# Optimization experiments

Hardware: AMD Instinct MI355X
Metric: run time of the kernel (lower is better)

## Reference

```python
import jax, jax.numpy as jnp
import numpy as np
import math

EPS = 1e-5
V_TH = 1.0


def heaviside(u):
    return (u >= 0.0).astype(u.dtype)


def setup_inputs() -> dict:
    key = jax.random.key(0)
    ks = jax.random.split(key, 8)
    N, C, T = 1024, 80, 500
    Cp1 = C + 1  # conv height: C + 2*32 - 64 + 1
    num_classes = 3
    x = jax.random.normal(ks[0], (N, C, T), dtype=jnp.float32)
    # Conv2d(1,1,(64,1)) params
    fan_in = 64 * 1
    bound = 1.0 / math.sqrt(fan_in)
    conv_w = jax.random.uniform(ks[1], (1, 1, 64, 1), jnp.float32, -bound, bound)
    conv_b = jax.random.uniform(ks[2], (1,), jnp.float32, -bound, bound)
    # BatchNorm1d(81), eval mode
    bn_gamma = jnp.ones((Cp1,), jnp.float32)
    bn_beta = jnp.zeros((Cp1,), jnp.float32)
    bn_mean = jax.random.normal(ks[3], (Cp1,), jnp.float32) * 0.1
    bn_var = jax.random.uniform(ks[4], (Cp1,), jnp.float32, 0.5, 1.5)
    # PLIF learnable time constant: tau = exp(-0.5)+1 -> w = -log(tau-1) = 0.5
    plif_w = jnp.asarray(0.5, jnp.float32)
    # Linear(81 -> 3)
    bnd = 1.0 / math.sqrt(Cp1)
    fc_w = jax.random.uniform(ks[5], (num_classes, Cp1), jnp.float32, -bnd, bnd)
    fc_b = jax.random.uniform(ks[6], (num_classes,), jnp.float32, -bnd, bnd)
    return {"x": x, "conv_w": conv_w, "conv_b": conv_b, "bn_gamma": bn_gamma,
            "bn_beta": bn_beta, "bn_mean": bn_mean, "bn_var": bn_var,
            "plif_w": plif_w, "fc_w": fc_w, "fc_b": fc_b}


def reference(x, conv_w, conv_b, bn_gamma, bn_beta, bn_mean, bn_var, plif_w, fc_w, fc_b):
    # x: (N, C, T) -> (N, 1, C, T), conv kernel (64,1) with padding (32,0) -> height C+1
    y = jax.lax.conv_general_dilated(x[:, None], conv_w, window_strides=(1, 1),
                                     padding=((32, 32), (0, 0)))
    y = y + conv_b[None, :, None, None]
    y = y[:, 0]  # (N, C+1, T)
    # BatchNorm1d (eval): per-channel affine normalize
    inv = bn_gamma / jnp.sqrt(bn_var + EPS)
    y = y * inv[None, :, None] + (bn_beta - bn_mean * inv)[None, :, None]
    seq = jnp.transpose(y, (2, 0, 1))  # (T, N, C+1)
    decay = jax.nn.sigmoid(plif_w)  # 1/tau
    v0 = jnp.zeros(seq.shape[1:], seq.dtype)

    def step(v, xt):
        v = v + (xt - v) * decay           # PLIF charge (decay_input, v_reset=0)
        s = heaviside(v - V_TH)            # fire
        v = v * (1.0 - s)                  # hard reset to 0
        return v, s

    _, spikes = jax.lax.scan(step, v0, seq)  # (T, N, C+1)
    feat = jnp.mean(spikes, axis=0)          # (N, C+1)
    out = feat @ fc_w.T + fc_b               # (N, num_classes); dropout = identity (eval)
    return out
```

## Files before the change

kernel.cpp:

```cpp
#include <hip/hip_runtime.h>
#include <math.h>


#define NTH      640
#define NFIR     512
#define CPW      11
#define TC       64
#define XROWS    151
#define YSTRIDE  65
#define NCHUNK   8
#define T_LEN    500
#define C_OUT    81

__global__ __launch_bounds__(NTH)
void snn_fused_ps_kernel(const float* __restrict__ x,
                         const float* __restrict__ conv_w,
                         const float* __restrict__ conv_b,
                         const float* __restrict__ bn_gamma,
                         const float* __restrict__ bn_beta,
                         const float* __restrict__ bn_mean,
                         const float* __restrict__ bn_var,
                         const float* __restrict__ plif_w,
                         const float* __restrict__ fc_w,
                         const float* __restrict__ fc_b,
                         float* __restrict__ out)
{
    __shared__ float xs[2][XROWS * TC];
    __shared__ float ybuf[2][C_OUT * YSTRIDE];
    __shared__ float wsh[64];
    __shared__ float feat[C_OUT];

    const int tid  = threadIdx.x;
    const int n    = blockIdx.x;
    const float* xn = x + (size_t)n * (80 * T_LEN);

    if (tid < 64) wsh[tid] = conv_w[tid];

    for (int i = tid; i < 32 * TC; i += NTH) { xs[0][i] = 0.0f; xs[1][i] = 0.0f; }
    for (int i = tid; i < (XROWS - 112) * TC; i += NTH) {
        xs[0][112 * TC + i] = 0.0f; xs[1][112 * TC + i] = 0.0f;
    }
    for (int i = tid; i < 1280; i += NTH) {
        const int cr = i >> 4, t4 = i & 15;
        float4 v4 = *reinterpret_cast<const float4*>(xn + cr * T_LEN + t4 * 4);
        *reinterpret_cast<float4*>(&xs[0][(cr + 32) * TC + t4 * 4]) = v4;
    }

    float v = 0.0f, cnt = 0.0f, inv_c = 0.0f, bb_c = 0.0f, decay = 0.0f;
    if (tid >= NFIR) {
        const int ch = tid - NFIR;
        decay = 1.0f / (1.0f + expf(-plif_w[0]));
        if (ch < C_OUT) {
            inv_c = bn_gamma[ch] * rsqrtf(bn_var[ch] + 1e-5f);
            bb_c  = conv_b[0] * inv_c + bn_beta[ch] - bn_mean[ch] * inv_c;
        }
    }
    __syncthreads();

    for (int c = 0; c < NCHUNK; ++c) {
        const int b = c & 1;

        if (tid < NFIR) {
            const int lane = tid & 63;
            const int co0  = (tid >> 6) * CPW;
            const float* xsb = xs[b];

            float acc[CPW];
            float win[CPW];
            #pragma unroll
            for (int r = 0; r < CPW; ++r) acc[r] = 0.0f;
            const int base = co0 * TC + lane;
            #pragma unroll
            for (int m = 0; m < CPW - 1; ++m) win[m] = xsb[base + m * TC];
            #pragma unroll
            for (int k = 0; k < 64; ++k) {
                win[(k + CPW - 1) % CPW] = xsb[base + (k + CPW - 1) * TC];
                const float wk = wsh[k];
                #pragma unroll
                for (int r = 0; r < CPW; ++r)
                    acc[r] = fmaf(wk, win[(k + r) % CPW], acc[r]);
            }
            #pragma unroll
            for (int r = 0; r < CPW; ++r) {
                const int co = co0 + r;
                if (co < C_OUT) ybuf[b][co * YSTRIDE + lane] = acc[r];
            }
        } else {
            const int sid = tid - NFIR;

            if (c < NCHUNK - 1) {
                const int t0n = (c + 1) * TC;
                float4 pf[10];
                #pragma unroll
                for (int s = 0; s < 10; ++s) {
                    const int i  = s * 128 + sid;
                    const int cr = i >> 4, t4 = i & 15;
                    int toff = t0n + t4 * 4;
                    if (toff > 496) toff = 496;
                    pf[s] = *reinterpret_cast<const float4*>(xn + cr * T_LEN + toff);
                }
                #pragma unroll
                for (int s = 0; s < 10; ++s) {
                    const int i  = s * 128 + sid;
                    const int cr = i >> 4, t4 = i & 15;
                    *reinterpret_cast<float4*>(&xs[b ^ 1][(cr + 32) * TC + t4 * 4]) = pf[s];
                }
            }

            if (c > 0 && sid < C_OUT) {
                const float* yrow = &ybuf[b ^ 1][sid * YSTRIDE];
                #pragma unroll 4
                for (int t = 0; t < TC; ++t) {
                    const float xt = fmaf(yrow[t], inv_c, bb_c);
                    v = fmaf(xt - v, decay, v);
                    const bool s = (v >= 1.0f);
                    cnt += s ? 1.0f : 0.0f;
                    v = s ? 0.0f : v;
                }
            }
        }
        __syncthreads();
    }

    if (tid >= NFIR) {
        const int sid = tid - NFIR;
        if (sid < C_OUT) {
            const float* yrow = &ybuf[1][sid * YSTRIDE];
            #pragma unroll 4
            for (int t = 0; t < 52; ++t) {
                const float xt = fmaf(yrow[t], inv_c, bb_c);
                v = fmaf(xt - v, decay, v);
                const bool s = (v >= 1.0f);
                cnt += s ? 1.0f : 0.0f;
                v = s ? 0.0f : v;
            }
            feat[sid] = cnt * (1.0f / 500.0f);
        }
    }
    __syncthreads();

    if (tid < 3) {
        float o = fc_b[tid];
        #pragma unroll 3
        for (int cc = 0; cc < C_OUT; ++cc)
            o = fmaf(feat[cc], fc_w[tid * C_OUT + cc], o);
        out[n * 3 + tid] = o;
    }
}

extern "C" void kernel_launch(void* const* d_in, const int* in_sizes, int n_in,
                              void* d_out, int out_size, void* d_ws, size_t ws_size,
                              hipStream_t stream)
{
    const float* x        = (const float*)d_in[0];
    const float* conv_w   = (const float*)d_in[1];
    const float* conv_b   = (const float*)d_in[2];
    const float* bn_gamma = (const float*)d_in[3];
    const float* bn_beta  = (const float*)d_in[4];
    const float* bn_mean  = (const float*)d_in[5];
    const float* bn_var   = (const float*)d_in[6];
    const float* plif_w   = (const float*)d_in[7];
    const float* fc_w     = (const float*)d_in[8];
    const float* fc_b     = (const float*)d_in[9];
    float* out            = (float*)d_out;

    snn_fused_ps_kernel<<<1024, NTH, 0, stream>>>(
        x, conv_w, conv_b, bn_gamma, bn_beta, bn_mean, bn_var,
        plif_w, fc_w, fc_b, out);
}
```

Baseline: 118.8 us.

## Retile conv to 60-step chunks with 14 outputs per thread and implicit zero padding

Changes the time chunk from 64 to 60 steps (9 chunks, 20-step tail), cuts the block from 640 to 512 threads with 6 FIR wavefronts each computing 14 output channels, and drops the zero-padding rows in shared memory in favour of bounds-checked loads. The goal is less shared memory per block and fewer wasted FIR wavefronts, which could let more blocks share a CU. In exchange each load carries a branch, 4 of the 64 lanes compute unused outputs, and the loop runs one more chunk with a serial scan per chunk.

```diff
diff --git a/kernel.cpp b/kernel.cpp
--- a/kernel.cpp
+++ b/kernel.cpp
@@ -2,48 +2,46 @@
 #include <math.h>
 
 
-#define NTH      640
-#define NFIR     512
-#define CPW      11
-#define TC       64
-#define XROWS    151
-#define YSTRIDE  65
-#define NCHUNK   8
+#define NTH      512
+#define NFIR     384
+#define CPW      14
+#define TC       60
+#define YSTRIDE  61
+#define NCHUNK   9
+#define TAIL     20
 #define T_LEN    500
 #define C_OUT    81
+#define NITEMS   1200
 
 __global__ __launch_bounds__(NTH)
-void snn_fused_ps_kernel(const float* __restrict__ x,
-                         const float* __restrict__ conv_w,
-                         const float* __restrict__ conv_b,
-                         const float* __restrict__ bn_gamma,
-                         const float* __restrict__ bn_beta,
-                         const float* __restrict__ bn_mean,
-                         const float* __restrict__ bn_var,
-                         const float* __restrict__ plif_w,
-                         const float* __restrict__ fc_w,
-                         const float* __restrict__ fc_b,
-                         float* __restrict__ out)
+void snn_ps5_kernel(const float* __restrict__ x,
+                    const float* __restrict__ conv_w,
+                    const float* __restrict__ conv_b,
+                    const float* __restrict__ bn_gamma,
+                    const float* __restrict__ bn_beta,
+                    const float* __restrict__ bn_mean,
+                    const float* __restrict__ bn_var,
+                    const float* __restrict__ plif_w,
+                    const float* __restrict__ fc_w,
+                    const float* __restrict__ fc_b,
+                    float* __restrict__ out)
 {
-    __shared__ float xs[2][XROWS * TC];
+    __shared__ float xs[2][80 * TC];
     __shared__ float ybuf[2][C_OUT * YSTRIDE];
     __shared__ float wsh[64];
     __shared__ float feat[C_OUT];
 
     const int tid  = threadIdx.x;
     const int n    = blockIdx.x;
+    const int lane = tid & 63;
     const float* xn = x + (size_t)n * (80 * T_LEN);
 
     if (tid < 64) wsh[tid] = conv_w[tid];
 
-    for (int i = tid; i < 32 * TC; i += NTH) { xs[0][i] = 0.0f; xs[1][i] = 0.0f; }
-    for (int i = tid; i < (XROWS - 112) * TC; i += NTH) {
-        xs[0][112 * TC + i] = 0.0f; xs[1][112 * TC + i] = 0.0f;
-    }
-    for (int i = tid; i < 1280; i += NTH) {
-        const int cr = i >> 4, t4 = i & 15;
+    for (int i = tid; i < NITEMS; i += NTH) {
+        const int cr = i / 15, t4 = i - cr * 15;
         float4 v4 = *reinterpret_cast<const float4*>(xn + cr * T_LEN + t4 * 4);
-        *reinterpret_cast<float4*>(&xs[0][(cr + 32) * TC + t4 * 4]) = v4;
+        *reinterpret_cast<float4*>(&xs[0][cr * TC + t4 * 4]) = v4;
     }
 
     float v = 0.0f, cnt = 0.0f, inv_c = 0.0f, bb_c = 0.0f, decay = 0.0f;
@@ -61,29 +59,34 @@
         const int b = c & 1;
 
         if (tid < NFIR) {
-            const int lane = tid & 63;
-            const int co0  = (tid >> 6) * CPW;
+            const int co0 = (tid >> 6) * CPW;
             const float* xsb = xs[b];
-
             float acc[CPW];
             float win[CPW];
             #pragma unroll
             for (int r = 0; r < CPW; ++r) acc[r] = 0.0f;
-            const int base = co0 * TC + lane;
+            const int row0 = co0 - 32;
             #pragma unroll
-            for (int m = 0; m < CPW - 1; ++m) win[m] = xsb[base + m * TC];
+            for (int m = 0; m < CPW - 1; ++m) {
+                const int row = row0 + m;
+                win[m] = ((unsigned)row < 80u) ? xsb[row * TC + lane] : 0.0f;
+            }
             #pragma unroll
             for (int k = 0; k < 64; ++k) {
-                win[(k + CPW - 1) % CPW] = xsb[base + (k + CPW - 1) * TC];
+                const int row = row0 + k + (CPW - 1);
+                win[(k + CPW - 1) % CPW] =
+                    ((unsigned)row < 80u) ? xsb[row * TC + lane] : 0.0f;
                 const float wk = wsh[k];
                 #pragma unroll
                 for (int r = 0; r < CPW; ++r)
                     acc[r] = fmaf(wk, win[(k + r) % CPW], acc[r]);
             }
-            #pragma unroll
-            for (int r = 0; r < CPW; ++r) {
-                const int co = co0 + r;
-                if (co < C_OUT) ybuf[b][co * YSTRIDE + lane] = acc[r];
+            if (lane < TC) {
+                #pragma unroll
+                for (int r = 0; r < CPW; ++r) {
+                    const int co = co0 + r;
+                    if (co < C_OUT) ybuf[b][co * YSTRIDE + lane] = acc[r];
+                }
             }
         } else {
             const int sid = tid - NFIR;
@@ -93,17 +96,21 @@
                 float4 pf[10];
                 #pragma unroll
                 for (int s = 0; s < 10; ++s) {
-                    const int i  = s * 128 + sid;
-                    const int cr = i >> 4, t4 = i & 15;
-                    int toff = t0n + t4 * 4;
-                    if (toff > 496) toff = 496;
-                    pf[s] = *reinterpret_cast<const float4*>(xn + cr * T_LEN + toff);
+                    const int i = s * 128 + sid;
+                    if (i < NITEMS) {
+                        const int cr = i / 15, t4 = i - cr * 15;
+                        int toff = t0n + t4 * 4;
+                        if (toff > 496) toff = 496;
+                        pf[s] = *reinterpret_cast<const float4*>(xn + cr * T_LEN + toff);
+                    }
                 }
                 #pragma unroll
                 for (int s = 0; s < 10; ++s) {
-                    const int i  = s * 128 + sid;
-                    const int cr = i >> 4, t4 = i & 15;
-                    *reinterpret_cast<float4*>(&xs[b ^ 1][(cr + 32) * TC + t4 * 4]) = pf[s];
+                    const int i = s * 128 + sid;
+                    if (i < NITEMS) {
+                        const int cr = i / 15, t4 = i - cr * 15;
+                        *reinterpret_cast<float4*>(&xs[b ^ 1][cr * TC + t4 * 4]) = pf[s];
+                    }
                 }
             }
 
@@ -125,9 +132,9 @@
     if (tid >= NFIR) {
         const int sid = tid - NFIR;
         if (sid < C_OUT) {
-            const float* yrow = &ybuf[1][sid * YSTRIDE];
+            const float* yrow = &ybuf[0][sid * YSTRIDE];
             #pragma unroll 4
-            for (int t = 0; t < 52; ++t) {
+            for (int t = 0; t < TAIL; ++t) {
                 const float xt = fmaf(yrow[t], inv_c, bb_c);
                 v = fmaf(xt - v, decay, v);
                 const bool s = (v >= 1.0f);
@@ -164,7 +171,7 @@
     const float* fc_b     = (const float*)d_in[9];
     float* out            = (float*)d_out;
 
-    snn_fused_ps_kernel<<<1024, NTH, 0, stream>>>(
+    snn_ps5_kernel<<<1024, NTH, 0, stream>>>(
         x, conv_w, conv_b, bn_gamma, bn_beta, bn_mean, bn_var,
         plif_w, fc_w, fc_b, out);
 }
```

After: 251.9 us. +112.0%, slower.
